# Optimization experiments

Hardware: AMD Instinct MI355X
Metric: run time of the kernel (lower is better)

Reference implementation:

```python
import jax, jax.numpy as jnp
import numpy as np
import math

IMG_COUNT = 5      # total_length = id_length + 1
NUM_TOKENS = 576   # (768//32)**2, the is_1024_resolution branch
CHANNELS = 1280
N_SEL = 288        # sa32 * NUM_TOKENS
HEADS = 20


def setup_inputs() -> dict:
    key = jax.random.key(0)
    ks = jax.random.split(key, 7)
    hidden_states = jax.random.normal(ks[0], (2 * IMG_COUNT, NUM_TOKENS, CHANNELS), dtype=jnp.float32)
    scale = 0.02
    Wq = jax.random.normal(ks[1], (CHANNELS, CHANNELS), dtype=jnp.float32) * scale
    Wk = jax.random.normal(ks[2], (CHANNELS, CHANNELS), dtype=jnp.float32) * scale
    Wv = jax.random.normal(ks[3], (CHANNELS, CHANNELS), dtype=jnp.float32) * scale
    Wo = jax.random.normal(ks[4], (CHANNELS, CHANNELS), dtype=jnp.float32) * scale
    bo = jnp.zeros((CHANNELS,), dtype=jnp.float32)
    # per-image random spatial token subsets (cal_attn_indice_xl_effcient_memory)
    indices = jax.random.randint(ks[5], (IMG_COUNT, N_SEL), 0, NUM_TOKENS, dtype=jnp.int64)
    return {"hidden_states": hidden_states, "Wq": Wq, "Wk": Wk, "Wv": Wv,
            "Wo": Wo, "bo": bo, "indices": indices, "heads": HEADS}


def _sdpa_block(q_in, kv_in, Wq, Wk, Wv, Wo, bo, heads):
    """Faithful __call2__: linear q/k/v, multi-head SDPA, output projection."""
    B, Tq, C = q_in.shape
    Tk = kv_in.shape[1]
    hd = C // heads
    q = (q_in @ Wq.T).reshape(B, Tq, heads, hd).transpose(0, 2, 1, 3)   # [B,H,Tq,hd]
    k = (kv_in @ Wk.T).reshape(B, Tk, heads, hd).transpose(0, 2, 1, 3)  # [B,H,Tk,hd]
    v = (kv_in @ Wv.T).reshape(B, Tk, heads, hd).transpose(0, 2, 1, 3)
    scale = 1.0 / math.sqrt(hd)
    scores = jnp.einsum('bhqd,bhkd->bhqk', q, k) * scale
    probs = jax.nn.softmax(scores, axis=-1)
    o = jnp.einsum('bhqk,bhkd->bhqd', probs, v)
    o = o.transpose(0, 2, 1, 3).reshape(B, Tq, C)
    return o @ Wo.T + bo


def reference(hidden_states, Wq, Wk, Wv, Wo, bo, indices, heads):
    B, T, C = hidden_states.shape
    P = indices.shape[0]          # img_count
    hs = hidden_states.reshape(2, P, T, C)
    # gathered[p] = hs[:, p, indices[p], :] -> [2, P, n_sel, C]
    gathered = hs[:, jnp.arange(P)[:, None], indices, :]
    outs = []
    for i in range(P):            # small fixed loop over images (structurally distinct KV banks)
        cur = hs[:, i]            # [2, T, C]
        others = jnp.concatenate([gathered[:, p] for p in range(P) if p != i], axis=1)
        enc = jnp.concatenate([others, cur], axis=1)  # [2, (P-1)*n_sel + T, C]
        outs.append(_sdpa_block(cur, enc, Wq, Wk, Wv, Wo, bo, heads))
    return jnp.stack(outs, axis=1).reshape(B, T, C)
```

## Files before the change

kernel.cpp:

```cpp
#include <hip/hip_runtime.h>

typedef __bf16 bf16_t;
typedef __attribute__((ext_vector_type(4))) __bf16 bf16x4;
typedef __attribute__((ext_vector_type(8))) __bf16 bf16x8;
typedef __attribute__((ext_vector_type(4))) float f32x4;

#define MFMA_BF16(a, b, c) __builtin_amdgcn_mfma_f32_16x16x32_bf16((a), (b), (c), 0, 0, 0)

namespace {

constexpr int PIMG  = 5;
constexpr int TTOK  = 576;
constexpr int CCH   = 1280;
constexpr int NSEL  = 288;
constexpr int NH    = 20;
constexpr int ROWS  = 2 * PIMG * TTOK;
constexpr int TKEYS = 4 * NSEL + TTOK;
constexpr int KT_TILES = TKEYS / 64;
constexpr size_t NXE = (size_t)ROWS * CCH;
constexpr size_t NWE = (size_t)CCH * CCH;

__device__ __forceinline__ bf16x8 cvt8(const float* p) {
  const float4 f0 = *(const float4*)p;
  const float4 f1 = *(const float4*)(p + 4);
  bf16x8 r;
  r[0] = (bf16_t)f0.x; r[1] = (bf16_t)f0.y; r[2] = (bf16_t)f0.z; r[3] = (bf16_t)f0.w;
  r[4] = (bf16_t)f1.x; r[5] = (bf16_t)f1.y; r[6] = (bf16_t)f1.z; r[7] = (bf16_t)f1.w;
  return r;
}

__global__ __launch_bounds__(256) void cvt_kernel(
    const float* __restrict__ X, const float* __restrict__ W0, const float* __restrict__ W1,
    const float* __restrict__ W2, const float* __restrict__ W3,
    bf16_t* __restrict__ Xb, bf16_t* __restrict__ Wb0, bf16_t* __restrict__ Wb1,
    bf16_t* __restrict__ Wb2, bf16_t* __restrict__ Wb3) {
  const int y = blockIdx.y;
  const float* src = y == 0 ? X : (y == 1 ? W0 : (y == 2 ? W1 : (y == 3 ? W2 : W3)));
  bf16_t* dst = y == 0 ? Xb : (y == 1 ? Wb0 : (y == 2 ? Wb1 : (y == 3 ? Wb2 : Wb3)));
  const size_t n = y == 0 ? NXE : NWE;
  const size_t idx = ((size_t)blockIdx.x * 256 + threadIdx.x) * 8;
  if (idx < n) *(bf16x8*)&dst[idx] = cvt8(&src[idx]);
}

template <bool BIAS, typename CT>
__device__ __forceinline__ void gemm_nt_body(const bf16_t* __restrict__ A,
                                             const bf16_t* __restrict__ B,
                                             const float* __restrict__ bias,
                                             CT* __restrict__ C,
                                             int bm, int bn, float scale) {
  constexpr int LDT = 72;
  __shared__ bf16_t As[128 * LDT];
  __shared__ bf16_t Bs[128 * LDT];

  const int tid  = threadIdx.x;
  const int lane = tid & 63;
  const int wave = tid >> 6;
  const int quad = lane >> 4;
  const int l16  = lane & 15;
  const int wr   = (wave >> 1) * 64;
  const int wc   = (wave & 1) * 64;
  const int m0   = bm * 128;
  const int n0   = bn * 128;
  const int srow = tid >> 3;
  const int scol = (tid & 7) * 8;

  bf16x8 pa[4], pb[4];
  auto loadAB = [&](int k0) {
#pragma unroll
    for (int p = 0; p < 4; ++p) {
      pa[p] = *(const bf16x8*)&A[(size_t)(m0 + srow + 32 * p) * CCH + k0 + scol];
      pb[p] = *(const bf16x8*)&B[(size_t)(n0 + srow + 32 * p) * CCH + k0 + scol];
    }
  };
  loadAB(0);

  f32x4 acc[4][4];
#pragma unroll
  for (int i = 0; i < 4; ++i)
#pragma unroll
    for (int j = 0; j < 4; ++j) acc[i][j] = (f32x4){0.f, 0.f, 0.f, 0.f};

  for (int it = 0; it < CCH / 64; ++it) {
#pragma unroll
    for (int p = 0; p < 4; ++p) {
      *(bf16x8*)&As[(srow + 32 * p) * LDT + scol] = pa[p];
      *(bf16x8*)&Bs[(srow + 32 * p) * LDT + scol] = pb[p];
    }
    __syncthreads();
    if (it < CCH / 64 - 1) loadAB((it + 1) * 64);
#pragma unroll
    for (int ks = 0; ks < 2; ++ks) {
      bf16x8 af[4], bfr[4];
#pragma unroll
      for (int i = 0; i < 4; ++i)
        af[i] = *(const bf16x8*)&As[(wr + 16 * i + l16) * LDT + ks * 32 + quad * 8];
#pragma unroll
      for (int j = 0; j < 4; ++j)
        bfr[j] = *(const bf16x8*)&Bs[(wc + 16 * j + l16) * LDT + ks * 32 + quad * 8];
#pragma unroll
      for (int i = 0; i < 4; ++i)
#pragma unroll
        for (int j = 0; j < 4; ++j)
          acc[i][j] = MFMA_BF16(af[i], bfr[j], acc[i][j]);
    }
    if (it < CCH / 64 - 1) __syncthreads();
  }

#pragma unroll
  for (int j = 0; j < 4; ++j) {
    const int col = n0 + wc + 16 * j + l16;
    const float bv = BIAS ? bias[col] : 0.f;
#pragma unroll
    for (int i = 0; i < 4; ++i) {
#pragma unroll
      for (int r = 0; r < 4; ++r) {
        const int row = m0 + wr + 16 * i + quad * 4 + r;
        const float val = acc[i][j][r] * scale + bv;
        if constexpr (sizeof(CT) == 2)
          C[(size_t)row * CCH + col] = (CT)val;
        else
          C[(size_t)row * CCH + col] = val;
      }
    }
  }
}

__global__ __launch_bounds__(256, 3) void qkv_gemm_kernel(
    const bf16_t* __restrict__ Xb,
    const bf16_t* __restrict__ Wqb, const bf16_t* __restrict__ Wkb, const bf16_t* __restrict__ Wvb,
    bf16_t* __restrict__ Qf, bf16_t* __restrict__ Kf, bf16_t* __restrict__ Vf) {
  const bf16_t* W = blockIdx.z == 0 ? Wqb : (blockIdx.z == 1 ? Wkb : Wvb);
  bf16_t* O = blockIdx.z == 0 ? Qf : (blockIdx.z == 1 ? Kf : Vf);
  const float scl = blockIdx.z == 0 ? 0.125f : 1.0f;
  gemm_nt_body<false, bf16_t>(Xb, W, nullptr, O, blockIdx.x, blockIdx.y, scl);
}

__global__ __launch_bounds__(256, 3) void out_gemm_kernel(
    const bf16_t* __restrict__ Of, const bf16_t* __restrict__ Wob,
    const float* __restrict__ bo, float* __restrict__ out) {
  gemm_nt_body<true, float>(Of, Wob, bo, out, blockIdx.x, blockIdx.y, 1.0f);
}

__global__ __launch_bounds__(256, 4) void attn_kernel(
    const bf16_t* __restrict__ Qf, const bf16_t* __restrict__ Kf, const bf16_t* __restrict__ Vf,
    const int* __restrict__ indices, bf16_t* __restrict__ Ofull) {
  __shared__ unsigned short kvrow[TKEYS];
  __shared__ bf16_t Vts[2][64 * 64];
  __shared__ bf16_t Ps[2][64 * 72];

  const int tid  = threadIdx.x;
  const int lane = tid & 63;
  const int wave = tid >> 6;
  const int quad = lane >> 4;
  const int l16  = lane & 15;

  const int b   = blockIdx.x;
  const int xcd = b & 7;
  const int t   = b >> 3;
  const int gi  = t / 9;
  const int qt  = t - gi * 9;
  const int g   = xcd + 8 * gi;
  const int h   = g % NH;
  const int si  = g / NH;
  const int s   = si / PIMG;
  const int ii  = si % PIMG;

  const int r0 = si * TTOK + qt * 64;
  const int hc = h * 64;

  bf16x8 aq[4][2];
#pragma unroll
  for (int n = 0; n < 4; ++n)
#pragma unroll
    for (int h2 = 0; h2 < 2; ++h2)
      aq[n][h2] = *(const bf16x8*)&Qf[(size_t)(r0 + 16 * n + l16) * CCH + hc + quad * 8 + 32 * h2];

  for (int j = tid; j < TKEYS; j += 256) {
    int row;
    if (j < 4 * NSEL) {
      const int jp = j / NSEL;
      const int jj = j - jp * NSEL;
      const int p  = jp + (jp >= ii ? 1 : 0);
      row = (s * PIMG + p) * TTOK + indices[p * NSEL + jj];
    } else {
      row = si * TTOK + (j - 4 * NSEL);
    }
    kvrow[j] = (unsigned short)row;
  }
  __syncthreads();

  const int jrow = tid >> 3;
  const int cdim = (tid & 7) * 8;

  bf16x8 kf0, kf1, vv0, vv1;
  bf16x8 nk0, nk1, nv0, nv1;
  auto load_tile = [&](int kt, bf16x8& a, bf16x8& b, bf16x8& c, bf16x8& d) {
    const int krow = kvrow[kt * 64 + 16 * wave + l16];
    a = *(const bf16x8*)&Kf[(size_t)krow * CCH + hc + quad * 8];
    b = *(const bf16x8*)&Kf[(size_t)krow * CCH + hc + quad * 8 + 32];
    const int ra = kvrow[kt * 64 + jrow];
    const int rb = kvrow[kt * 64 + jrow + 32];
    c = *(const bf16x8*)&Vf[(size_t)ra * CCH + hc + cdim];
    d = *(const bf16x8*)&Vf[(size_t)rb * CCH + hc + cdim];
  };
  load_tile(0, kf0, kf1, vv0, vv1);

  float l_part[4] = {0.f, 0.f, 0.f, 0.f};
  f32x4 oacc[4];
#pragma unroll
  for (int n = 0; n < 4; ++n) oacc[n] = (f32x4){0.f, 0.f, 0.f, 0.f};

  const int cb0 = jrow ^ cdim;
  const int cb1 = (jrow + 32) ^ cdim;

  for (int kt = 0; kt < KT_TILES; ++kt) {
    bf16_t* __restrict__ Vcur = &Vts[kt & 1][0];
    bf16_t* __restrict__ Pcur = &Ps[kt & 1][0];

    if (kt < KT_TILES - 1) load_tile(kt + 1, nk0, nk1, nv0, nv1);

#pragma unroll
    for (int x = 0; x < 8; ++x) {
      Vcur[(cdim + x) * 64 + cb0] = vv0[x];
      Vcur[(cdim + x) * 64 + cb1] = vv1[x];
    }

    f32x4 sacc[4];
#pragma unroll
    for (int n = 0; n < 4; ++n) {
      f32x4 z = (f32x4){0.f, 0.f, 0.f, 0.f};
      z = MFMA_BF16(kf0, aq[n][0], z);
      z = MFMA_BF16(kf1, aq[n][1], z);
      sacc[n] = z;
    }

#pragma unroll
    for (int n = 0; n < 4; ++n) {
      bf16x4 pb;
      float sum = 0.f;
#pragma unroll
      for (int r = 0; r < 4; ++r) {
        const float pv = __expf(sacc[n][r]);
        pb[r] = (bf16_t)pv;
        sum += pv;
      }
      l_part[n] += sum;
      *(bf16x4*)&Pcur[(16 * n + l16) * 72 + 16 * wave + 4 * quad] = pb;
    }

    __syncthreads();

    const bf16x8 vf0 = *(const bf16x8*)&Vcur[(16 * wave + l16) * 64 + ((quad * 8) ^ ((16 * wave + l16) & 56))];
    const bf16x8 vf1 = *(const bf16x8*)&Vcur[(16 * wave + l16) * 64 + ((quad * 8 + 32) ^ ((16 * wave + l16) & 56))];
#pragma unroll
    for (int n = 0; n < 4; ++n) {
      const bf16x8 pf0 = *(const bf16x8*)&Pcur[(16 * n + l16) * 72 + quad * 8];
      const bf16x8 pf1 = *(const bf16x8*)&Pcur[(16 * n + l16) * 72 + quad * 8 + 32];
      oacc[n] = MFMA_BF16(pf0, vf0, oacc[n]);
      oacc[n] = MFMA_BF16(pf1, vf1, oacc[n]);
    }

    kf0 = nk0; kf1 = nk1; vv0 = nv0; vv1 = nv1;
  }

  __syncthreads();

  float* lred = (float*)&Ps[0][0];
  float* linv = (float*)&Vts[0][0];
#pragma unroll
  for (int n = 0; n < 4; ++n)
    lred[(16 * n + l16) * 16 + 4 * wave + quad] = l_part[n];
  __syncthreads();
  if (tid < 64) {
    float tt = 0.f;
#pragma unroll
    for (int i = 0; i < 16; ++i) tt += lred[tid * 16 + i];
    linv[tid] = 1.f / tt;
  }
  __syncthreads();
#pragma unroll
  for (int n = 0; n < 4; ++n) {
#pragma unroll
    for (int r = 0; r < 4; ++r) {
      const int qloc = 16 * n + 4 * quad + r;
      Ofull[(size_t)(r0 + qloc) * CCH + hc + 16 * wave + l16] =
          (bf16_t)(oacc[n][r] * linv[qloc]);
    }
  }
}

}

extern "C" void kernel_launch(void* const* d_in, const int* in_sizes, int n_in,
                              void* d_out, int out_size, void* d_ws, size_t ws_size,
                              hipStream_t stream) {
  const float* hs = (const float*)d_in[0];
  const float* Wq = (const float*)d_in[1];
  const float* Wk = (const float*)d_in[2];
  const float* Wv = (const float*)d_in[3];
  const float* Wo = (const float*)d_in[4];
  const float* bo = (const float*)d_in[5];
  const int* indices = (const int*)d_in[6];
  float* out = (float*)d_out;

  bf16_t* Qf  = (bf16_t*)d_ws;
  bf16_t* Kf  = Qf + NXE;
  bf16_t* Vf  = Kf + NXE;
  bf16_t* Xb  = Vf + NXE;
  bf16_t* Of  = Xb;
  bf16_t* Wqb = Xb + NXE;
  bf16_t* Wkb = Wqb + NWE;
  bf16_t* Wvb = Wkb + NWE;
  bf16_t* Wob = Wvb + NWE;

  dim3 g0((NXE + 2047) / 2048, 5);
  cvt_kernel<<<g0, dim3(256), 0, stream>>>(hs, Wq, Wk, Wv, Wo, Xb, Wqb, Wkb, Wvb, Wob);

  dim3 g1(ROWS / 128, CCH / 128, 3);
  qkv_gemm_kernel<<<g1, dim3(256), 0, stream>>>(Xb, Wqb, Wkb, Wvb, Qf, Kf, Vf);

  attn_kernel<<<dim3(1800), dim3(256), 0, stream>>>(Qf, Kf, Vf, indices, Of);

  dim3 g3(ROWS / 128, CCH / 128, 1);
  out_gemm_kernel<<<g3, dim3(256), 0, stream>>>(Of, Wob, bo, out);
}
```

Before: 320.0 us.

## Deepen K/V global prefetch to two tiles ahead with triple register buffers

```diff
diff --git a/kernel.cpp b/kernel.cpp
--- a/kernel.cpp
+++ b/kernel.cpp
@@ -191,46 +191,46 @@
 
   const int jrow = tid >> 3;
   const int cdim = (tid & 7) * 8;
-
-  bf16x8 kf0, kf1, vv0, vv1;
-  bf16x8 nk0, nk1, nv0, nv1;
-  auto load_tile = [&](int kt, bf16x8& a, bf16x8& b, bf16x8& c, bf16x8& d) {
+  const int cb0 = jrow ^ cdim;
+  const int cb1 = (jrow + 32) ^ cdim;
+
+  auto load_tile = [&](int kt, bf16x8 (&T)[4]) {
     const int krow = kvrow[kt * 64 + 16 * wave + l16];
-    a = *(const bf16x8*)&Kf[(size_t)krow * CCH + hc + quad * 8];
-    b = *(const bf16x8*)&Kf[(size_t)krow * CCH + hc + quad * 8 + 32];
+    T[0] = *(const bf16x8*)&Kf[(size_t)krow * CCH + hc + quad * 8];
+    T[1] = *(const bf16x8*)&Kf[(size_t)krow * CCH + hc + quad * 8 + 32];
     const int ra = kvrow[kt * 64 + jrow];
     const int rb = kvrow[kt * 64 + jrow + 32];
-    c = *(const bf16x8*)&Vf[(size_t)ra * CCH + hc + cdim];
-    d = *(const bf16x8*)&Vf[(size_t)rb * CCH + hc + cdim];
+    T[2] = *(const bf16x8*)&Vf[(size_t)ra * CCH + hc + cdim];
+    T[3] = *(const bf16x8*)&Vf[(size_t)rb * CCH + hc + cdim];
   };
-  load_tile(0, kf0, kf1, vv0, vv1);
+
+  bf16x8 TA[4], TB[4], TC[4];
+  load_tile(0, TA);
+  load_tile(1, TB);
 
   float l_part[4] = {0.f, 0.f, 0.f, 0.f};
   f32x4 oacc[4];
 #pragma unroll
   for (int n = 0; n < 4; ++n) oacc[n] = (f32x4){0.f, 0.f, 0.f, 0.f};
 
-  const int cb0 = jrow ^ cdim;
-  const int cb1 = (jrow + 32) ^ cdim;
-
-  for (int kt = 0; kt < KT_TILES; ++kt) {
+  auto body = [&](int kt, bf16x8 (&CUR)[4], bf16x8 (&FUT)[4]) {
+    if (kt + 2 < KT_TILES) load_tile(kt + 2, FUT);
+
     bf16_t* __restrict__ Vcur = &Vts[kt & 1][0];
     bf16_t* __restrict__ Pcur = &Ps[kt & 1][0];
 
-    if (kt < KT_TILES - 1) load_tile(kt + 1, nk0, nk1, nv0, nv1);
-
 #pragma unroll
     for (int x = 0; x < 8; ++x) {
-      Vcur[(cdim + x) * 64 + cb0] = vv0[x];
-      Vcur[(cdim + x) * 64 + cb1] = vv1[x];
+      Vcur[(cdim + x) * 64 + cb0] = CUR[2][x];
+      Vcur[(cdim + x) * 64 + cb1] = CUR[3][x];
     }
 
     f32x4 sacc[4];
 #pragma unroll
     for (int n = 0; n < 4; ++n) {
       f32x4 z = (f32x4){0.f, 0.f, 0.f, 0.f};
-      z = MFMA_BF16(kf0, aq[n][0], z);
-      z = MFMA_BF16(kf1, aq[n][1], z);
+      z = MFMA_BF16(CUR[0], aq[n][0], z);
+      z = MFMA_BF16(CUR[1], aq[n][1], z);
       sacc[n] = z;
     }
 
@@ -248,7 +248,9 @@
       *(bf16x4*)&Pcur[(16 * n + l16) * 72 + 16 * wave + 4 * quad] = pb;
     }
 
-    __syncthreads();
+    asm volatile("s_waitcnt lgkmcnt(0)" ::: "memory");
+    __builtin_amdgcn_s_barrier();
+    asm volatile("" ::: "memory");
 
     const bf16x8 vf0 = *(const bf16x8*)&Vcur[(16 * wave + l16) * 64 + ((quad * 8) ^ ((16 * wave + l16) & 56))];
     const bf16x8 vf1 = *(const bf16x8*)&Vcur[(16 * wave + l16) * 64 + ((quad * 8 + 32) ^ ((16 * wave + l16) & 56))];
@@ -259,8 +261,12 @@
       oacc[n] = MFMA_BF16(pf0, vf0, oacc[n]);
       oacc[n] = MFMA_BF16(pf1, vf1, oacc[n]);
     }
-
-    kf0 = nk0; kf1 = nk1; vv0 = nv0; vv1 = nv1;
+  };
+
+  for (int base = 0; base < KT_TILES; base += 3) {
+    body(base + 0, TA, TC);
+    body(base + 1, TB, TA);
+    body(base + 2, TC, TB);
   }
 
   __syncthreads();
```

New measurement: 598.1 us. +86.9%, slower.

## Give each wave its own query rows and keep P in registers

Applied to the files above, without the earlier changes.

```diff
diff --git a/kernel.cpp b/kernel.cpp
--- a/kernel.cpp
+++ b/kernel.cpp
@@ -146,7 +146,6 @@
     const int* __restrict__ indices, bf16_t* __restrict__ Ofull) {
   __shared__ unsigned short kvrow[TKEYS];
   __shared__ bf16_t Vts[2][64 * 64];
-  __shared__ bf16_t Ps[2][64 * 72];
 
   const int tid  = threadIdx.x;
   const int lane = tid & 63;
@@ -168,12 +167,8 @@
   const int r0 = si * TTOK + qt * 64;
   const int hc = h * 64;
 
-  bf16x8 aq[4][2];
-#pragma unroll
-  for (int n = 0; n < 4; ++n)
-#pragma unroll
-    for (int h2 = 0; h2 < 2; ++h2)
-      aq[n][h2] = *(const bf16x8*)&Qf[(size_t)(r0 + 16 * n + l16) * CCH + hc + quad * 8 + 32 * h2];
+  const bf16x8 aq0 = *(const bf16x8*)&Qf[(size_t)(r0 + 16 * wave + l16) * CCH + hc + quad * 8];
+  const bf16x8 aq1 = *(const bf16x8*)&Qf[(size_t)(r0 + 16 * wave + l16) * CCH + hc + quad * 8 + 32];
 
   for (int j = tid; j < TKEYS; j += 256) {
     int row;
@@ -189,103 +184,99 @@
   }
   __syncthreads();
 
+  const int chi  = ((l16 & 12) << 1) | (l16 & 3);
   const int jrow = tid >> 3;
   const int cdim = (tid & 7) * 8;
 
-  bf16x8 kf0, kf1, vv0, vv1;
-  bf16x8 nk0, nk1, nv0, nv1;
-  auto load_tile = [&](int kt, bf16x8& a, bf16x8& b, bf16x8& c, bf16x8& d) {
-    const int krow = kvrow[kt * 64 + 16 * wave + l16];
-    a = *(const bf16x8*)&Kf[(size_t)krow * CCH + hc + quad * 8];
-    b = *(const bf16x8*)&Kf[(size_t)krow * CCH + hc + quad * 8 + 32];
-    const int ra = kvrow[kt * 64 + jrow];
-    const int rb = kvrow[kt * 64 + jrow + 32];
+  auto load_v = [&](int kt, bf16x8& c, bf16x8& d) {
+    const unsigned int pr = *(const unsigned int*)&kvrow[kt * 64 + 2 * jrow];
+    const int ra = pr & 0xffff;
+    const int rb = pr >> 16;
     c = *(const bf16x8*)&Vf[(size_t)ra * CCH + hc + cdim];
     d = *(const bf16x8*)&Vf[(size_t)rb * CCH + hc + cdim];
   };
-  load_tile(0, kf0, kf1, vv0, vv1);
-
-  float l_part[4] = {0.f, 0.f, 0.f, 0.f};
+
+  bf16x8 cv0, cv1, nv0, nv1;
+  load_v(0, cv0, cv1);
+
+  float lsum = 0.f;
   f32x4 oacc[4];
 #pragma unroll
-  for (int n = 0; n < 4; ++n) oacc[n] = (f32x4){0.f, 0.f, 0.f, 0.f};
-
-  const int cb0 = jrow ^ cdim;
-  const int cb1 = (jrow + 32) ^ cdim;
+  for (int dg = 0; dg < 4; ++dg) oacc[dg] = (f32x4){0.f, 0.f, 0.f, 0.f};
 
   for (int kt = 0; kt < KT_TILES; ++kt) {
-    bf16_t* __restrict__ Vcur = &Vts[kt & 1][0];
-    bf16_t* __restrict__ Pcur = &Ps[kt & 1][0];
-
-    if (kt < KT_TILES - 1) load_tile(kt + 1, nk0, nk1, nv0, nv1);
-
-#pragma unroll
-    for (int x = 0; x < 8; ++x) {
-      Vcur[(cdim + x) * 64 + cb0] = vv0[x];
-      Vcur[(cdim + x) * 64 + cb1] = vv1[x];
-    }
+    {
+      unsigned int* V32 = (unsigned int*)&Vts[kt & 1][0];
+      const unsigned short* s0 = (const unsigned short*)&cv0;
+      const unsigned short* s1 = (const unsigned short*)&cv1;
+#pragma unroll
+      for (int x = 0; x < 8; ++x) {
+        const int col2 = jrow ^ ((cdim ^ (x << 3)) >> 1);
+        V32[(cdim + x) * 32 + col2] = (unsigned int)s0[x] | ((unsigned int)s1[x] << 16);
+      }
+    }
+
+    if (kt + 1 < KT_TILES) load_v(kt + 1, nv0, nv1);
 
     f32x4 sacc[4];
 #pragma unroll
-    for (int n = 0; n < 4; ++n) {
+    for (int kg = 0; kg < 4; ++kg) {
+      const int koff = (kg >> 1) * 32 + (kg & 1) * 4;
+      const int krow = kvrow[kt * 64 + koff + chi];
+      const bf16x8 kf0 = *(const bf16x8*)&Kf[(size_t)krow * CCH + hc + quad * 8];
+      const bf16x8 kf1 = *(const bf16x8*)&Kf[(size_t)krow * CCH + hc + quad * 8 + 32];
       f32x4 z = (f32x4){0.f, 0.f, 0.f, 0.f};
-      z = MFMA_BF16(kf0, aq[n][0], z);
-      z = MFMA_BF16(kf1, aq[n][1], z);
-      sacc[n] = z;
-    }
-
-#pragma unroll
-    for (int n = 0; n < 4; ++n) {
-      bf16x4 pb;
-      float sum = 0.f;
+      z = MFMA_BF16(kf0, aq0, z);
+      z = MFMA_BF16(kf1, aq1, z);
+      sacc[kg] = z;
+    }
+
+    bf16x8 pa0, pa1;
+    float ls = 0.f;
+#pragma unroll
+    for (int kg = 0; kg < 4; ++kg) {
 #pragma unroll
       for (int r = 0; r < 4; ++r) {
-        const float pv = __expf(sacc[n][r]);
-        pb[r] = (bf16_t)pv;
-        sum += pv;
+        const float pv = __expf(sacc[kg][r]);
+        ls += pv;
+        const int e = (kg & 1) * 4 + r;
+        if (kg < 2) pa0[e] = (bf16_t)pv;
+        else        pa1[e] = (bf16_t)pv;
       }
-      l_part[n] += sum;
-      *(bf16x4*)&Pcur[(16 * n + l16) * 72 + 16 * wave + 4 * quad] = pb;
-    }
+    }
+    lsum += ls;
 
     __syncthreads();
 
-    const bf16x8 vf0 = *(const bf16x8*)&Vcur[(16 * wave + l16) * 64 + ((quad * 8) ^ ((16 * wave + l16) & 56))];
-    const bf16x8 vf1 = *(const bf16x8*)&Vcur[(16 * wave + l16) * 64 + ((quad * 8 + 32) ^ ((16 * wave + l16) & 56))];
-#pragma unroll
-    for (int n = 0; n < 4; ++n) {
-      const bf16x8 pf0 = *(const bf16x8*)&Pcur[(16 * n + l16) * 72 + quad * 8];
-      const bf16x8 pf1 = *(const bf16x8*)&Pcur[(16 * n + l16) * 72 + quad * 8 + 32];
-      oacc[n] = MFMA_BF16(pf0, vf0, oacc[n]);
-      oacc[n] = MFMA_BF16(pf1, vf1, oacc[n]);
-    }
-
-    kf0 = nk0; kf1 = nk1; vv0 = nv0; vv1 = nv1;
+    const bf16_t* __restrict__ Vb = &Vts[kt & 1][0];
+#pragma unroll
+    for (int dg = 0; dg < 4; ++dg) {
+      const int d  = 16 * dg + l16;
+      const int sw = (d & 56) ^ ((d & 7) << 3);
+      const bf16x8 vf0 = *(const bf16x8*)&Vb[d * 64 + ((8 * quad) ^ sw)];
+      const bf16x8 vf1 = *(const bf16x8*)&Vb[d * 64 + ((32 + 8 * quad) ^ sw)];
+      oacc[dg] = MFMA_BF16(pa0, vf0, oacc[dg]);
+      oacc[dg] = MFMA_BF16(pa1, vf1, oacc[dg]);
+    }
+
+    cv0 = nv0; cv1 = nv1;
   }
 
   __syncthreads();
 
-  float* lred = (float*)&Ps[0][0];
-  float* linv = (float*)&Vts[0][0];
-#pragma unroll
-  for (int n = 0; n < 4; ++n)
-    lred[(16 * n + l16) * 16 + 4 * wave + quad] = l_part[n];
+  float* lred = (float*)&Vts[0][0];
+  lred[(16 * wave + l16) * 4 + quad] = lsum;
   __syncthreads();
-  if (tid < 64) {
-    float tt = 0.f;
-#pragma unroll
-    for (int i = 0; i < 16; ++i) tt += lred[tid * 16 + i];
-    linv[tid] = 1.f / tt;
-  }
-  __syncthreads();
-#pragma unroll
-  for (int n = 0; n < 4; ++n) {
-#pragma unroll
-    for (int r = 0; r < 4; ++r) {
-      const int qloc = 16 * n + 4 * quad + r;
-      Ofull[(size_t)(r0 + qloc) * CCH + hc + 16 * wave + l16] =
-          (bf16_t)(oacc[n][r] * linv[qloc]);
-    }
+#pragma unroll
+  for (int r = 0; r < 4; ++r) {
+    const int qloc = 16 * wave + 4 * quad + r;
+    const float tt = lred[qloc * 4 + 0] + lred[qloc * 4 + 1] +
+                     lred[qloc * 4 + 2] + lred[qloc * 4 + 3];
+    const float inv = 1.f / tt;
+#pragma unroll
+    for (int dg = 0; dg < 4; ++dg)
+      Ofull[(size_t)(r0 + qloc) * CCH + hc + 16 * dg + l16] =
+          (bf16_t)(oacc[dg][r] * inv);
   }
 }
 
```

After: 419.6 us. 31.1% more time.
